# Optimization experiments

Hardware: AMD Instinct MI355X
Metric: run time of the kernel (lower is better)

The kernel has to match this reference:

```python
import jax, jax.numpy as jnp
import numpy as np

B, S, H, W, L = 32, 512, 768, 256, 8  # batch, subword seq, hidden, max words, max group size
INTENT, SLOT = 26, 121


def setup_inputs() -> dict:
    key = jax.random.key(0)
    ks = jax.random.split(key, 16)
    sc = 0.02
    res_all = jax.random.normal(ks[0], (B, S, H), jnp.float32)
    res = jax.random.normal(ks[1], (B, H), jnp.float32)
    # group covers indices start..start+lens inclusive (lens+1 <= L elements)
    token_start_idxs = jax.random.randint(ks[2], (B, W), 0, S - L, jnp.int32)
    subword_lengths = jax.random.randint(ks[3], (B, W), 1, L, jnp.int32)  # 1..7
    return {
        'res_all': res_all,
        'res': res,
        'token_start_idxs': token_start_idxs,
        'subword_lengths': subword_lengths,
        'Wsq_w': jax.random.normal(ks[4], (H, H), jnp.float32) * sc,
        'Wsq_b': jnp.zeros((H,), jnp.float32),
        'Wsk_w': jax.random.normal(ks[5], (H, H), jnp.float32) * sc,
        'Wsk_b': jnp.zeros((H,), jnp.float32),
        'Wsv_w': jax.random.normal(ks[6], (H, H), jnp.float32) * sc,
        'Wsv_b': jnp.zeros((H,), jnp.float32),
        'lin_id_w': jax.random.normal(ks[7], (INTENT, H), jnp.float32) * sc,
        'lin_id_b': jnp.zeros((INTENT,), jnp.float32),
        'lin_slot_w': jax.random.normal(ks[8], (SLOT, H), jnp.float32) * sc,
        'lin_slot_b': jnp.zeros((SLOT,), jnp.float32),
    }


def reference(res_all, res, token_start_idxs, subword_lengths,
              Wsq_w, Wsq_b, Wsk_w, Wsk_b, Wsv_w, Wsv_b,
              lin_id_w, lin_id_b, lin_slot_w, lin_slot_b):
    # intent head on pooled output
    res_id = res @ lin_id_w.T + lin_id_b  # [B, INTENT]

    # gather padded subword groups: torch.range is inclusive -> lens+1 subwords
    offs = jnp.arange(L, dtype=jnp.int32)                        # [L]
    idx = token_start_idxs[:, :, None] + offs[None, None, :]     # [B, W, L]
    idx = jnp.clip(idx, 0, S - 1)
    group = res_all[jnp.arange(B)[:, None, None], idx]           # [B, W, L, H]
    valid = offs[None, None, :] <= subword_lengths[:, :, None]   # [B, W, L], lens+1 valid

    # SAA_Attn: only the first row's attention output is used
    q0 = group[:, :, 0, :] @ Wsq_w.T + Wsq_b                     # [B, W, H]
    K = group @ Wsk_w.T + Wsk_b                                  # [B, W, L, H]
    V = group @ Wsv_w.T + Wsv_b                                  # [B, W, L, H]
    scores = jnp.einsum('bwh,bwkh->bwk', q0, K)                  # [B, W, L]
    scores = jnp.where(valid, scores, jnp.float32(-1e9))
    attn = jax.nn.softmax(scores, axis=-1)
    first = group[:, :, 0, :]
    attn_word = jnp.einsum('bwk,bwkh->bwh', attn, V) + first     # [B, W, H]

    # lens == 1 branch bypasses attention entirely
    word = jnp.where((subword_lengths == 1)[:, :, None], first, attn_word)

    res_sf = word @ lin_slot_w.T + lin_slot_b                    # [B, W, SLOT]
    return res_id, res_sf
```

## Files before the change

### kernel.cpp

```cpp
#include <hip/hip_runtime.h>
#include <cstdint>
#include <cstddef>

#define BB 32
#define SS 512
#define HH 768
#define WW 256
#define LL 8
#define NINTENT 26
#define NSLOT 121

typedef float f32x4 __attribute__((ext_vector_type(4)));
typedef __bf16 bf16x8 __attribute__((ext_vector_type(8)));

static __device__ __forceinline__ float bf2f(unsigned short u) {
    union { unsigned int i; float f; } x; x.i = ((unsigned int)u) << 16; return x.f;
}
static __device__ __forceinline__ unsigned short f2bf(float f) {
    union { float f; unsigned int i; } x; x.f = f;
    unsigned int r = (x.i + 0x7fffu + ((x.i >> 16) & 1u)) >> 16;
    return (unsigned short)r;
}

static __device__ __forceinline__ void gload16(const void* g, void* l) {
    __builtin_amdgcn_global_load_lds(
        (const __attribute__((address_space(1))) void*)g,
        (__attribute__((address_space(3))) void*)l, 16, 0, 0);
}

#define MF(a, b, c) __builtin_amdgcn_mfma_f32_16x16x32_bf16((a), (b), (c), 0, 0, 0)

__global__ __launch_bounds__(256) void prep_w(
    const float* __restrict__ Wk, const float* __restrict__ Wq,
    const float* __restrict__ Wv, const float* __restrict__ Ws,
    const float* __restrict__ bq, const float* __restrict__ bv,
    unsigned short* __restrict__ WkT_hi, unsigned short* __restrict__ WkT_lo,
    unsigned short* __restrict__ WqT_hi, unsigned short* __restrict__ WqT_lo,
    unsigned short* __restrict__ WvT, unsigned short* __restrict__ Wcomb,
    float* __restrict__ u_part,
    float* __restrict__ wsbv_part)
{
    int bid = blockIdx.x;
    int t = threadIdx.x;

    if (bid < 432) {
        __shared__ float tl[64][65];
        int mb = bid / 144, tb = bid % 144;
        int tx = tb % 12, ty = tb / 12;
        const float* src = (mb == 0) ? Wk : (mb == 1) ? Wq : Wv;
        int rr = t >> 4, c4 = (t & 15) * 4;
#pragma unroll
        for (int j = 0; j < 4; j++) {
            float4 v = *reinterpret_cast<const float4*>(
                &src[(size_t)(ty * 64 + rr + 16 * j) * HH + tx * 64 + c4]);
            tl[rr + 16 * j][c4 + 0] = v.x; tl[rr + 16 * j][c4 + 1] = v.y;
            tl[rr + 16 * j][c4 + 2] = v.z; tl[rr + 16 * j][c4 + 3] = v.w;
        }
        __syncthreads();
        int il = t >> 4, o4 = (t & 15) * 4;
        unsigned short* dhi = (mb == 0) ? WkT_hi : (mb == 1) ? WqT_hi : WvT;
        unsigned short* dlo = (mb == 0) ? WkT_lo : WqT_lo;
#pragma unroll
        for (int j = 0; j < 4; j++) {
            int i = il + 16 * j;
            float v0 = tl[o4 + 0][i], v1 = tl[o4 + 1][i];
            float v2 = tl[o4 + 2][i], v3 = tl[o4 + 3][i];
            size_t off = (size_t)(tx * 64 + i) * HH + ty * 64 + o4;
            ushort4 h;
            h.x = f2bf(v0); h.y = f2bf(v1); h.z = f2bf(v2); h.w = f2bf(v3);
            *reinterpret_cast<ushort4*>(&dhi[off]) = h;
            if (mb < 2) {
                ushort4 l;
                l.x = f2bf(v0 - bf2f(h.x)); l.y = f2bf(v1 - bf2f(h.y));
                l.z = f2bf(v2 - bf2f(h.z)); l.w = f2bf(v3 - bf2f(h.w));
                *reinterpret_cast<ushort4*>(&dlo[off]) = l;
            }
        }
        if (mb == 0) {
            int c = t >> 2, q = t & 3;
            float s = 0.f;
#pragma unroll
            for (int r = 0; r < 16; r++)
                s += bq[ty * 64 + q * 16 + r] * tl[q * 16 + r][c];
            s += __shfl_xor(s, 1);
            s += __shfl_xor(s, 2);
            if (q == 0) u_part[ty * HH + tx * 64 + c] = s;
        }
    } else {
        __shared__ float wred[4];
        int bid2 = bid - 432;
        int idx = bid2 * 256 + t;
        int row = idx / HH, col = idx % HH;
        float v = (row < NSLOT) ? Ws[row * HH + col] : 0.f;
        Wcomb[row * 1536 + col] = f2bf(v);
        float pv = v * bv[col];
        int lane = t & 63, wave = t >> 6;
#pragma unroll
        for (int off = 32; off > 0; off >>= 1) pv += __shfl_xor(pv, off);
        if (lane == 0) wred[wave] = pv;
        __syncthreads();
        if (t == 0)
            wsbv_part[(bid2 % 3) * 128 + row] = wred[0] + wred[1] + wred[2] + wred[3];
    }
}

__global__ __launch_bounds__(256) void gemm_weights(
    const uint4* __restrict__ WkT_hi, const uint4* __restrict__ WkT_lo,
    const uint4* __restrict__ WqT_hi, const uint4* __restrict__ WqT_lo,
    const uint4* __restrict__ WvT, const uint4* __restrict__ Wcomb,
    const float* __restrict__ res_all, const int* __restrict__ starts,
    const float* __restrict__ res, const float* __restrict__ id_w,
    const float* __restrict__ id_b,
    float* __restrict__ Ppart,
    float* __restrict__ WRpart,
    unsigned short* __restrict__ slotA,
    float* __restrict__ out)
{
    __shared__ uint4 sA[512];
    __shared__ uint4 sB[512];
    int bid = blockIdx.x;
    int t = threadIdx.x;
    int lane = t & 63, wave = t >> 6;

    if (bid >= 2384) {
        int w = (bid - 2384) * 4 + wave;
        int bb = w / 26, o = w - bb * 26;
        const float* rrow = res + bb * HH + lane * 12;
        const float* wrow = id_w + o * HH + lane * 12;
        float s = 0.f;
#pragma unroll
        for (int c = 0; c < 3; c++) {
            float4 a = *reinterpret_cast<const float4*>(&rrow[c * 4]);
            float4 b = *reinterpret_cast<const float4*>(&wrow[c * 4]);
            s += a.x * b.x + a.y * b.y + a.z * b.z + a.w * b.w;
        }
#pragma unroll
        for (int off = 32; off > 0; off >>= 1) s += __shfl_xor(s, off);
        if (lane == 0) out[bb * NINTENT + o] = s + id_b[o];
        return;
    }
    if (bid >= 336) {
        int gw = (bid - 336) * 4 + wave;
        int b = gw >> 8;
        int s0 = starts[gw];
        const float* src = res_all + (size_t)(b * SS + s0) * HH + lane * 12;
        unsigned short* dst = slotA + (size_t)gw * 1536 + lane * 12;
#pragma unroll
        for (int c2 = 0; c2 < 3; c2++) {
            float4 v = *reinterpret_cast<const float4*>(&src[c2 * 4]);
            ushort4 o;
            o.x = f2bf(v.x); o.y = f2bf(v.y); o.z = f2bf(v.z); o.w = f2bf(v.w);
            *reinterpret_cast<ushort4*>(&dst[c2 * 4]) = o;
        }
        return;
    }

    int wm = wave >> 1, wn = wave & 1;
    int l16 = lane & 15, lk = lane >> 4;
    int srow = lane >> 2, schk = lane & 3;
    uint4* sA0 = &sA[wave * 128];
    uint4* sA1 = &sA[wave * 128 + 64];
    uint4* sB0 = &sB[wave * 128];
    uint4* sB1 = &sB[wave * 128 + 64];

    f32x4 acc[4][4] = {};

    if (bid < 288) {
        int tile = bid >> 3, ks = bid & 7;
        int mt = tile / 6, nt = tile % 6;
        int kb = ks * 12;
#pragma unroll
        for (int p = 0; p < 3; p++) {
            const uint4* Ab = (p == 1) ? WkT_lo : WkT_hi;
            const uint4* Bb = (p == 2) ? WqT_lo : WqT_hi;
            const uint4* Ag0 = Ab + (size_t)(mt * 128 + wave * 32 + srow) * 96 + kb + schk;
            const uint4* Ag1 = Ag0 + (size_t)16 * 96;
            const uint4* Bg0 = Bb + (size_t)(nt * 128 + wave * 32 + srow) * 96 + kb + schk;
            const uint4* Bg1 = Bg0 + (size_t)16 * 96;
            for (int k0 = 0; k0 < 12; k0 += 4) {
                gload16(Ag0 + k0, sA0); gload16(Ag1 + k0, sA1);
                gload16(Bg0 + k0, sB0); gload16(Bg1 + k0, sB1);
                __syncthreads();
                bf16x8 af[4], bfr[4];
#pragma unroll
                for (int i = 0; i < 4; i++)
                    af[i] = *reinterpret_cast<const bf16x8*>(&sA[(wm * 64 + i * 16 + l16) * 4 + lk]);
#pragma unroll
                for (int j = 0; j < 4; j++)
                    bfr[j] = *reinterpret_cast<const bf16x8*>(&sB[(wn * 64 + j * 16 + l16) * 4 + lk]);
#pragma unroll
                for (int i = 0; i < 4; i++)
#pragma unroll
                    for (int j = 0; j < 4; j++)
                        acc[i][j] = MF(af[i], bfr[j], acc[i][j]);
                __syncthreads();
            }
        }
        float* dst = Ppart + (size_t)ks * 589824;
#pragma unroll
        for (int i = 0; i < 4; i++)
#pragma unroll
            for (int j = 0; j < 4; j++) {
                int col = nt * 128 + wn * 64 + j * 16 + l16;
#pragma unroll
                for (int q = 0; q < 4; q++) {
                    int row = mt * 128 + wm * 64 + i * 16 + lk * 4 + q;
                    dst[(size_t)row * HH + col] = acc[i][j][q];
                }
            }
    } else {
        int idx = bid - 288;
        int nt = idx >> 3, ks = idx & 7;
        int kb = ks * 12;
        const uint4* Ag0 = Wcomb + (size_t)(wave * 32 + srow) * 192 + kb + schk;
        const uint4* Ag1 = Ag0 + (size_t)16 * 192;
        const uint4* Bg0 = WvT + (size_t)(nt * 128 + wave * 32 + srow) * 96 + kb + schk;
        const uint4* Bg1 = Bg0 + (size_t)16 * 96;
        for (int k0 = 0; k0 < 12; k0 += 4) {
            gload16(Ag0 + k0, sA0); gload16(Ag1 + k0, sA1);
            gload16(Bg0 + k0, sB0); gload16(Bg1 + k0, sB1);
            __syncthreads();
            bf16x8 af[4], bfr[4];
#pragma unroll
            for (int i = 0; i < 4; i++)
                af[i] = *reinterpret_cast<const bf16x8*>(&sA[(wm * 64 + i * 16 + l16) * 4 + lk]);
#pragma unroll
            for (int j = 0; j < 4; j++)
                bfr[j] = *reinterpret_cast<const bf16x8*>(&sB[(wn * 64 + j * 16 + l16) * 4 + lk]);
#pragma unroll
            for (int i = 0; i < 4; i++)
#pragma unroll
                for (int j = 0; j < 4; j++)
                    acc[i][j] = MF(af[i], bfr[j], acc[i][j]);
            __syncthreads();
        }
        float* dst = WRpart + (size_t)ks * 98304;
#pragma unroll
        for (int i = 0; i < 4; i++)
#pragma unroll
            for (int j = 0; j < 4; j++) {
                int col = nt * 128 + wn * 64 + j * 16 + l16;
#pragma unroll
                for (int q = 0; q < 4; q++) {
                    int row = wm * 64 + i * 16 + lk * 4 + q;
                    dst[(size_t)row * HH + col] = acc[i][j][q];
                }
            }
    }
}

__global__ __launch_bounds__(256) void psum_kernel(
    const float4* __restrict__ Ppart, ushort4* __restrict__ Pb,
    const float4* __restrict__ WRpart, unsigned short* __restrict__ Wcomb,
    const float* __restrict__ u_part, float* __restrict__ u,
    const float* __restrict__ wsbv_part, float* __restrict__ wsbv)
{
    int bid = blockIdx.x, t = threadIdx.x;
    if (bid < 576) {
        int i = bid * 256 + t;
        float4 s = Ppart[i];
#pragma unroll
        for (int k = 1; k < 8; k++) {
            float4 v = Ppart[(size_t)k * 147456 + i];
            s.x += v.x; s.y += v.y; s.z += v.z; s.w += v.w;
        }
        ushort4 o;
        o.x = f2bf(s.x); o.y = f2bf(s.y); o.z = f2bf(s.z); o.w = f2bf(s.w);
        Pb[i] = o;
    } else if (bid < 672) {
        int q = (bid - 576) * 256 + t;
        float4 s = WRpart[q];
#pragma unroll
        for (int k = 1; k < 8; k++) {
            float4 v = WRpart[(size_t)k * 24576 + q];
            s.x += v.x; s.y += v.y; s.z += v.z; s.w += v.w;
        }
        int row = q / 192, colq = q % 192;
        ushort4 o;
        o.x = f2bf(s.x); o.y = f2bf(s.y); o.z = f2bf(s.z); o.w = f2bf(s.w);
        *reinterpret_cast<ushort4*>(&Wcomb[row * 1536 + 768 + colq * 4]) = o;
    } else if (bid < 675) {
        int c = (bid - 672) * 256 + t;
        float s = 0.f;
#pragma unroll
        for (int ty = 0; ty < 12; ty++) s += u_part[ty * HH + c];
        u[c] = s;
    } else if (t < 128) {
        wsbv[t] = wsbv_part[t] + wsbv_part[128 + t] + wsbv_part[256 + t];
    }
}

__global__ __launch_bounds__(256) void gemm_qp_sl(
    const uint4* __restrict__ A,
    const uint4* __restrict__ Bm,
    const uint4* __restrict__ Wc,
    const float* __restrict__ u,
    float* __restrict__ qp,
    float* __restrict__ Cpart0)
{
    __shared__ uint4 sA[256];
    __shared__ uint4 sB[512];

    int bid = blockIdx.x;
    int t = threadIdx.x;
    int lane = t & 63, wave = t >> 6;
    int wm = wave >> 1, wn = wave & 1;
    int l16 = lane & 15, lk = lane >> 4;
    int srow = lane >> 2, schk = lane & 3;

    if (bid >= 768) {
        int mt = bid - 768;
        const uint4* Ag  = A + (size_t)(mt * 32 + wave * 16 + srow) * 192 + schk;
        const uint4* Bg0 = Wc + (size_t)(wave * 32 + srow) * 192 + schk;
        const uint4* Bg1 = Bg0 + (size_t)16 * 192;
        uint4* sB0 = &sB[wave * 128];
        uint4* sB1 = &sB[wave * 128 + 64];

        f32x4 acc[4] = {};
        for (int k0 = 0; k0 < 96; k0 += 4) {
            if (wave < 2) gload16(Ag + k0, &sA[wave * 64]);
            gload16(Bg0 + k0, sB0);
            gload16(Bg1 + k0, sB1);
            __syncthreads();
            bf16x8 af = *reinterpret_cast<const bf16x8*>(&sA[(wm * 16 + l16) * 4 + lk]);
            bf16x8 bfr[4];
#pragma unroll
            for (int j = 0; j < 4; j++)
                bfr[j] = *reinterpret_cast<const bf16x8*>(&sB[(wn * 64 + j * 16 + l16) * 4 + lk]);
#pragma unroll
            for (int j = 0; j < 4; j++)
                acc[j] = MF(af, bfr[j], acc[j]);
            __syncthreads();
        }
#pragma unroll
        for (int j = 0; j < 4; j++) {
            int col = wn * 64 + j * 16 + l16;
#pragma unroll
            for (int q = 0; q < 4; q++) {
                int row = mt * 32 + wm * 16 + lk * 4 + q;
                Cpart0[(size_t)row * 128 + col] = acc[j][q];
            }
        }
        return;
    }

    bid = (bid & 7) * 96 + (bid >> 3);
    int mt = bid / 6, nt = bid % 6;

    const uint4* Ag  = A + (size_t)(mt * 64 + wave * 16 + srow) * 192 + schk;
    const uint4* Bg0 = Bm + (size_t)(nt * 128 + wave * 32 + srow) * 96 + schk;
    const uint4* Bg1 = Bg0 + (size_t)16 * 96;
    uint4* sAp = &sA[wave * 64];
    uint4* sB0 = &sB[wave * 128];
    uint4* sB1 = &sB[wave * 128 + 64];

    f32x4 acc[2][4] = {};

    for (int k0 = 0; k0 < 96; k0 += 4) {
        gload16(Ag + k0, sAp);
        gload16(Bg0 + k0, sB0);
        gload16(Bg1 + k0, sB1);
        __syncthreads();
        bf16x8 af[2], bfr[4];
#pragma unroll
        for (int i = 0; i < 2; i++)
            af[i] = *reinterpret_cast<const bf16x8*>(&sA[(wm * 32 + i * 16 + l16) * 4 + lk]);
#pragma unroll
        for (int j = 0; j < 4; j++)
            bfr[j] = *reinterpret_cast<const bf16x8*>(&sB[(wn * 64 + j * 16 + l16) * 4 + lk]);
#pragma unroll
        for (int i = 0; i < 2; i++)
#pragma unroll
            for (int j = 0; j < 4; j++)
                acc[i][j] = MF(af[i], bfr[j], acc[i][j]);
        __syncthreads();
    }

#pragma unroll
    for (int i = 0; i < 2; i++)
#pragma unroll
        for (int j = 0; j < 4; j++) {
            int col = nt * 128 + wn * 64 + j * 16 + l16;
            float add = u[col];
#pragma unroll
            for (int q = 0; q < 4; q++) {
                int row = mt * 64 + wm * 32 + i * 16 + lk * 4 + q;
                qp[(size_t)row * HH + col] = acc[i][j][q] + add;
            }
        }
}

__global__ __launch_bounds__(256) void attn2_kernel(
    const float* __restrict__ qp,
    const float* __restrict__ res_all,
    const int* __restrict__ starts,
    const int* __restrict__ lens,
    unsigned short* __restrict__ slotA)
{
    int bid = blockIdx.x;
    bid = (bid & 7) * 256 + (bid >> 3);
    int gw = bid * 4 + (threadIdx.x >> 6);
    int lane = threadIdx.x & 63;
    int b = gw >> 8;
    int s0 = starts[gw];
    int sl = lens[gw];

    unsigned short* dst = slotA + (size_t)gw * 1536 + 768 + lane * 12;

    if (sl == 1) {
        ushort4 z = {0, 0, 0, 0};
#pragma unroll
        for (int c = 0; c < 3; c++) *reinterpret_cast<ushort4*>(&dst[c * 4]) = z;
        return;
    }

    const float* qrow = qp + (size_t)gw * HH + lane * 12;
    float q[12];
#pragma unroll
    for (int c = 0; c < 3; c++) {
        float4 v = *reinterpret_cast<const float4*>(&qrow[c * 4]);
        q[c * 4 + 0] = v.x; q[c * 4 + 1] = v.y; q[c * 4 + 2] = v.z; q[c * 4 + 3] = v.w;
    }

    float m = -1e30f, ssum = 0.f;
    float acc[12];
#pragma unroll
    for (int i = 0; i < 12; i++) acc[i] = 0.f;

    for (int k = 0; k < LL; k++) {
        if (k > sl) break;
        int s = s0 + k; if (s > SS - 1) s = SS - 1;
        const float* xr = res_all + (size_t)(b * SS + s) * HH + lane * 12;
        float x[12];
        float partial = 0.f;
#pragma unroll
        for (int c = 0; c < 3; c++) {
            float4 v = *reinterpret_cast<const float4*>(&xr[c * 4]);
            x[c * 4 + 0] = v.x; x[c * 4 + 1] = v.y;
            x[c * 4 + 2] = v.z; x[c * 4 + 3] = v.w;
            partial += q[c * 4 + 0] * v.x + q[c * 4 + 1] * v.y
                     + q[c * 4 + 2] * v.z + q[c * 4 + 3] * v.w;
        }
#pragma unroll
        for (int off = 32; off > 0; off >>= 1) partial += __shfl_xor(partial, off);

        float mnew = (partial > m) ? partial : m;
        float scale = __expf(m - mnew);
        float e = __expf(partial - mnew);
        ssum = ssum * scale + e;
#pragma unroll
        for (int i = 0; i < 12; i++) acc[i] = acc[i] * scale + e * x[i];
        m = mnew;
    }

    float inv = 1.f / ssum;
#pragma unroll
    for (int c = 0; c < 3; c++) {
        ushort4 o;
        o.x = f2bf(acc[c * 4 + 0] * inv); o.y = f2bf(acc[c * 4 + 1] * inv);
        o.z = f2bf(acc[c * 4 + 2] * inv); o.w = f2bf(acc[c * 4 + 3] * inv);
        *reinterpret_cast<ushort4*>(&dst[c * 4]) = o;
    }
}

__global__ __launch_bounds__(256) void gemm_slot_r(
    const uint4* __restrict__ A,
    const uint4* __restrict__ Bm,
    const float* __restrict__ Cpart0,
    const float* __restrict__ bias, const float* __restrict__ wsbv,
    const int* __restrict__ lens,
    float* __restrict__ outsf)
{
    __shared__ uint4 sA[128];
    __shared__ uint4 sB[512];

    int mt = blockIdx.x;
    int t = threadIdx.x;
    int lane = t & 63, wave = t >> 6;
    int wm = wave >> 1, wn = wave & 1;
    int l16 = lane & 15, lk = lane >> 4;
    int srow = lane >> 2, schk = lane & 3;

    const uint4* Ag  = A + (size_t)(mt * 32 + wave * 16 + srow) * 192 + 96 + schk;
    const uint4* Bg0 = Bm + (size_t)(wave * 32 + srow) * 192 + 96 + schk;
    const uint4* Bg1 = Bg0 + (size_t)16 * 192;
    uint4* sB0 = &sB[wave * 128];
    uint4* sB1 = &sB[wave * 128 + 64];

    f32x4 acc[4] = {};

    for (int k0 = 0; k0 < 96; k0 += 4) {
        if (wave < 2) gload16(Ag + k0, &sA[wave * 64]);
        gload16(Bg0 + k0, sB0);
        gload16(Bg1 + k0, sB1);
        __syncthreads();
        bf16x8 af = *reinterpret_cast<const bf16x8*>(&sA[(wm * 16 + l16) * 4 + lk]);
        bf16x8 bfr[4];
#pragma unroll
        for (int j = 0; j < 4; j++)
            bfr[j] = *reinterpret_cast<const bf16x8*>(&sB[(wn * 64 + j * 16 + l16) * 4 + lk]);
#pragma unroll
        for (int j = 0; j < 4; j++)
            acc[j] = MF(af, bfr[j], acc[j]);
        __syncthreads();
    }

#pragma unroll
    for (int j = 0; j < 4; j++) {
        int col = wn * 64 + j * 16 + l16;
        if (col < NSLOT) {
            float bc = bias[col], wv = wsbv[col];
#pragma unroll
            for (int q = 0; q < 4; q++) {
                int row = mt * 32 + wm * 16 + lk * 4 + q;
                float v = acc[j][q] + Cpart0[(size_t)row * 128 + col]
                        + bc + ((lens[row] > 1) ? wv : 0.f);
                outsf[(size_t)row * NSLOT + col] = v;
            }
        }
    }
}

extern "C" void kernel_launch(void* const* d_in, const int* in_sizes, int n_in,
                              void* d_out, int out_size, void* d_ws, size_t ws_size,
                              hipStream_t stream) {
    const float* res_all    = (const float*)d_in[0];
    const float* res        = (const float*)d_in[1];
    const int*   starts     = (const int*)d_in[2];
    const int*   lens       = (const int*)d_in[3];
    const float* Wsq_w      = (const float*)d_in[4];
    const float* Wsq_b      = (const float*)d_in[5];
    const float* Wsk_w      = (const float*)d_in[6];
    const float* Wsk_b      = (const float*)d_in[7];
    const float* Wsv_w      = (const float*)d_in[8];
    const float* Wsv_b      = (const float*)d_in[9];
    const float* lin_id_w   = (const float*)d_in[10];
    const float* lin_id_b   = (const float*)d_in[11];
    const float* lin_slot_w = (const float*)d_in[12];
    const float* lin_slot_b = (const float*)d_in[13];
    float* out = (float*)d_out;
    (void)Wsk_b;

    char* ws = (char*)d_ws;
    unsigned short* slotA     = (unsigned short*)(ws + 0);
    float*          qp        = (float*)(ws + 25165824);
    unsigned short* WkT_hi    = (unsigned short*)(ws + 50331648);
    unsigned short* WkT_lo    = (unsigned short*)(ws + 51511296);
    unsigned short* WqT_hi    = (unsigned short*)(ws + 52690944);
    unsigned short* WqT_lo    = (unsigned short*)(ws + 53870592);
    unsigned short* WvT       = (unsigned short*)(ws + 55050240);
    unsigned short* Pb        = (unsigned short*)(ws + 56229888);
    unsigned short* Wcomb     = (unsigned short*)(ws + 57409536);
    float*          u         = (float*)(ws + 57802752);
    float*          wsbv      = (float*)(ws + 57805824);
    float*          u_part    = (float*)(ws + 57806336);
    float*          wsbv_part = (float*)(ws + 57843200);
    float*          Ppart     = (float*)(ws + 57845760);
    float*          WRpart    = (float*)(ws + 76720128);
    float*          Cpart0    = (float*)(ws + 79865856);

    prep_w<<<816, 256, 0, stream>>>(
        Wsk_w, Wsq_w, Wsv_w, lin_slot_w, Wsq_b, Wsv_b,
        WkT_hi, WkT_lo, WqT_hi, WqT_lo, WvT, Wcomb,
        u_part, wsbv_part);

    gemm_weights<<<2592, 256, 0, stream>>>(
        (const uint4*)WkT_hi, (const uint4*)WkT_lo,
        (const uint4*)WqT_hi, (const uint4*)WqT_lo,
        (const uint4*)WvT, (const uint4*)Wcomb,
        res_all, starts, res, lin_id_w, lin_id_b,
        Ppart, WRpart, slotA, out);

    psum_kernel<<<676, 256, 0, stream>>>(
        (const float4*)Ppart, (ushort4*)Pb, (const float4*)WRpart, Wcomb,
        u_part, u, wsbv_part, wsbv);

    gemm_qp_sl<<<1024, 256, 0, stream>>>((const uint4*)slotA, (const uint4*)Pb,
                                         (const uint4*)Wcomb, u, qp, Cpart0);

    attn2_kernel<<<2048, 256, 0, stream>>>(qp, res_all, starts, lens, slotA);

    gemm_slot_r<<<256, 256, 0, stream>>>((const uint4*)slotA, (const uint4*)Wcomb,
                                         Cpart0, lin_slot_b, wsbv, lens, out + 832);
}
```

Before: 88.31 us.

## Shrink weight-GEMM tiles, move slot GEMM into psum kernel, store qp in bf16

The weight-precompute GEMM tiles drop from 128x128 to 64x64. This gives four times more blocks for better occupancy and load balance, at the cost of lower data reuse per block. The slot-projection partial GEMM moves out of the qp GEMM and into the psum kernel launch, so it runs alongside the reductions. The qp intermediate is now stored as bf16, which halves its write and read traffic but loses some query precision in the attention scores.

Result: slower. 92.66 us (+4.9%).

```diff
diff --git a/kernel.cpp b/kernel.cpp
--- a/kernel.cpp
+++ b/kernel.cpp
@@ -116,14 +116,14 @@
     unsigned short* __restrict__ slotA,
     float* __restrict__ out)
 {
-    __shared__ uint4 sA[512];
-    __shared__ uint4 sB[512];
+    __shared__ uint4 sA[256];
+    __shared__ uint4 sB[256];
     int bid = blockIdx.x;
     int t = threadIdx.x;
     int lane = t & 63, wave = t >> 6;
 
-    if (bid >= 2384) {
-        int w = (bid - 2384) * 4 + wave;
+    if (bid >= 3392) {
+        int w = (bid - 3392) * 4 + wave;
         int bb = w / 26, o = w - bb * 26;
         const float* rrow = res + bb * HH + lane * 12;
         const float* wrow = id_w + o * HH + lane * 12;
@@ -139,8 +139,8 @@
         if (lane == 0) out[bb * NINTENT + o] = s + id_b[o];
         return;
     }
-    if (bid >= 336) {
-        int gw = (bid - 336) * 4 + wave;
+    if (bid >= 1344) {
+        int gw = (bid - 1344) * 4 + wave;
         int b = gw >> 8;
         int s0 = starts[gw];
         const float* src = res_all + (size_t)(b * SS + s0) * HH + lane * 12;
@@ -158,91 +158,84 @@
     int wm = wave >> 1, wn = wave & 1;
     int l16 = lane & 15, lk = lane >> 4;
     int srow = lane >> 2, schk = lane & 3;
-    uint4* sA0 = &sA[wave * 128];
-    uint4* sA1 = &sA[wave * 128 + 64];
-    uint4* sB0 = &sB[wave * 128];
-    uint4* sB1 = &sB[wave * 128 + 64];
-
-    f32x4 acc[4][4] = {};
-
-    if (bid < 288) {
+
+    f32x4 acc[2][2] = {};
+
+    if (bid < 1152) {
         int tile = bid >> 3, ks = bid & 7;
-        int mt = tile / 6, nt = tile % 6;
+        int mt = tile / 12, nt = tile % 12;
         int kb = ks * 12;
 #pragma unroll
         for (int p = 0; p < 3; p++) {
             const uint4* Ab = (p == 1) ? WkT_lo : WkT_hi;
             const uint4* Bb = (p == 2) ? WqT_lo : WqT_hi;
-            const uint4* Ag0 = Ab + (size_t)(mt * 128 + wave * 32 + srow) * 96 + kb + schk;
-            const uint4* Ag1 = Ag0 + (size_t)16 * 96;
-            const uint4* Bg0 = Bb + (size_t)(nt * 128 + wave * 32 + srow) * 96 + kb + schk;
-            const uint4* Bg1 = Bg0 + (size_t)16 * 96;
+            const uint4* Ag = Ab + (size_t)(mt * 64 + wave * 16 + srow) * 96 + kb + schk;
+            const uint4* Bg = Bb + (size_t)(nt * 64 + wave * 16 + srow) * 96 + kb + schk;
             for (int k0 = 0; k0 < 12; k0 += 4) {
-                gload16(Ag0 + k0, sA0); gload16(Ag1 + k0, sA1);
-                gload16(Bg0 + k0, sB0); gload16(Bg1 + k0, sB1);
+                gload16(Ag + k0, &sA[wave * 64]);
+                gload16(Bg + k0, &sB[wave * 64]);
                 __syncthreads();
-                bf16x8 af[4], bfr[4];
-#pragma unroll
-                for (int i = 0; i < 4; i++)
-                    af[i] = *reinterpret_cast<const bf16x8*>(&sA[(wm * 64 + i * 16 + l16) * 4 + lk]);
-#pragma unroll
-                for (int j = 0; j < 4; j++)
-                    bfr[j] = *reinterpret_cast<const bf16x8*>(&sB[(wn * 64 + j * 16 + l16) * 4 + lk]);
-#pragma unroll
-                for (int i = 0; i < 4; i++)
-#pragma unroll
-                    for (int j = 0; j < 4; j++)
+                bf16x8 af[2], bfr[2];
+#pragma unroll
+                for (int i = 0; i < 2; i++)
+                    af[i] = *reinterpret_cast<const bf16x8*>(&sA[(wm * 32 + i * 16 + l16) * 4 + lk]);
+#pragma unroll
+                for (int j = 0; j < 2; j++)
+                    bfr[j] = *reinterpret_cast<const bf16x8*>(&sB[(wn * 32 + j * 16 + l16) * 4 + lk]);
+#pragma unroll
+                for (int i = 0; i < 2; i++)
+#pragma unroll
+                    for (int j = 0; j < 2; j++)
                         acc[i][j] = MF(af[i], bfr[j], acc[i][j]);
                 __syncthreads();
             }
         }
         float* dst = Ppart + (size_t)ks * 589824;
 #pragma unroll
-        for (int i = 0; i < 4; i++)
-#pragma unroll
-            for (int j = 0; j < 4; j++) {
-                int col = nt * 128 + wn * 64 + j * 16 + l16;
+        for (int i = 0; i < 2; i++)
+#pragma unroll
+            for (int j = 0; j < 2; j++) {
+                int col = nt * 64 + wn * 32 + j * 16 + l16;
 #pragma unroll
                 for (int q = 0; q < 4; q++) {
-                    int row = mt * 128 + wm * 64 + i * 16 + lk * 4 + q;
+                    int row = mt * 64 + wm * 32 + i * 16 + lk * 4 + q;
                     dst[(size_t)row * HH + col] = acc[i][j][q];
                 }
             }
     } else {
-        int idx = bid - 288;
-        int nt = idx >> 3, ks = idx & 7;
+        int idx = bid - 1152;
+        int tile = idx >> 3, ks = idx & 7;
+        int mt = tile / 12, nt = tile % 12;
         int kb = ks * 12;
-        const uint4* Ag0 = Wcomb + (size_t)(wave * 32 + srow) * 192 + kb + schk;
-        const uint4* Ag1 = Ag0 + (size_t)16 * 192;
-        const uint4* Bg0 = WvT + (size_t)(nt * 128 + wave * 32 + srow) * 96 + kb + schk;
-        const uint4* Bg1 = Bg0 + (size_t)16 * 96;
+        const uint4* Ag = Wcomb + (size_t)(mt * 64 + wave * 16 + srow) * 192 + kb + schk;
+        const uint4* Bg = WvT + (size_t)(nt * 64 + wave * 16 + srow) * 96 + kb + schk;
         for (int k0 = 0; k0 < 12; k0 += 4) {
-            gload16(Ag0 + k0, sA0); gload16(Ag1 + k0, sA1);
-            gload16(Bg0 + k0, sB0); gload16(Bg1 + k0, sB1);
+            gload16(Ag + k0, &sA[wave * 64]);
+            gload16(Bg + k0, &sB[wave * 64]);
             __syncthreads();
-            bf16x8 af[4], bfr[4];
-#pragma unroll
-            for (int i = 0; i < 4; i++)
-                af[i] = *reinterpret_cast<const bf16x8*>(&sA[(wm * 64 + i * 16 + l16) * 4 + lk]);
-#pragma unroll
-            for (int j = 0; j < 4; j++)
-                bfr[j] = *reinterpret_cast<const bf16x8*>(&sB[(wn * 64 + j * 16 + l16) * 4 + lk]);
-#pragma unroll
-            for (int i = 0; i < 4; i++)
-#pragma unroll
-                for (int j = 0; j < 4; j++)
+            bf16x8 af[2], bfr[2];
+#pragma unroll
+            for (int i = 0; i < 2; i++)
+                af[i] = *reinterpret_cast<const bf16x8*>(&sA[(wm * 32 + i * 16 + l16) * 4 + lk]);
+#pragma unroll
+            for (int j = 0; j < 2; j++)
+                bfr[j] = *reinterpret_cast<const bf16x8*>(&sB[(wn * 32 + j * 16 + l16) * 4 + lk]);
+#pragma unroll
+            for (int i = 0; i < 2; i++)
+#pragma unroll
+                for (int j = 0; j < 2; j++)
                     acc[i][j] = MF(af[i], bfr[j], acc[i][j]);
             __syncthreads();
         }
         float* dst = WRpart + (size_t)ks * 98304;
 #pragma unroll
-        for (int i = 0; i < 4; i++)
-#pragma unroll
-            for (int j = 0; j < 4; j++) {
-                int col = nt * 128 + wn * 64 + j * 16 + l16;
+        for (int i = 0; i < 2; i++)
+#pragma unroll
+            for (int j = 0; j < 2; j++) {
+                int col = nt * 64 + wn * 32 + j * 16 + l16;
 #pragma unroll
                 for (int q = 0; q < 4; q++) {
-                    int row = wm * 64 + i * 16 + lk * 4 + q;
+                    int row = mt * 64 + wm * 32 + i * 16 + lk * 4 + q;
                     dst[(size_t)row * HH + col] = acc[i][j][q];
                 }
             }
@@ -253,8 +246,13 @@
     const float4* __restrict__ Ppart, ushort4* __restrict__ Pb,
     const float4* __restrict__ WRpart, unsigned short* __restrict__ Wcomb,
     const float* __restrict__ u_part, float* __restrict__ u,
-    const float* __restrict__ wsbv_part, float* __restrict__ wsbv)
+    const float* __restrict__ wsbv_part, float* __restrict__ wsbv,
+    const uint4* __restrict__ A,
+    const uint4* __restrict__ Wc,
+    float* __restrict__ Cpart0)
 {
+    __shared__ uint4 sA[128];
+    __shared__ uint4 sB[512];
     int bid = blockIdx.x, t = threadIdx.x;
     if (bid < 576) {
         int i = bid * 256 + t;
@@ -285,31 +283,16 @@
 #pragma unroll
         for (int ty = 0; ty < 12; ty++) s += u_part[ty * HH + c];
         u[c] = s;
-    } else if (t < 128) {
-        wsbv[t] = wsbv_part[t] + wsbv_part[128 + t] + wsbv_part[256 + t];
-    }
-}
-
-__global__ __launch_bounds__(256) void gemm_qp_sl(
-    const uint4* __restrict__ A,
-    const uint4* __restrict__ Bm,
-    const uint4* __restrict__ Wc,
-    const float* __restrict__ u,
-    float* __restrict__ qp,
-    float* __restrict__ Cpart0)
-{
-    __shared__ uint4 sA[256];
-    __shared__ uint4 sB[512];
-
-    int bid = blockIdx.x;
-    int t = threadIdx.x;
-    int lane = t & 63, wave = t >> 6;
-    int wm = wave >> 1, wn = wave & 1;
-    int l16 = lane & 15, lk = lane >> 4;
-    int srow = lane >> 2, schk = lane & 3;
-
-    if (bid >= 768) {
-        int mt = bid - 768;
+    } else if (bid == 675) {
+        if (t < 128)
+            wsbv[t] = wsbv_part[t] + wsbv_part[128 + t] + wsbv_part[256 + t];
+    } else {
+        int mt = bid - 676;
+        int lane = t & 63, wave = t >> 6;
+        int wm = wave >> 1, wn = wave & 1;
+        int l16 = lane & 15, lk = lane >> 4;
+        int srow = lane >> 2, schk = lane & 3;
+
         const uint4* Ag  = A + (size_t)(mt * 32 + wave * 16 + srow) * 192 + schk;
         const uint4* Bg0 = Wc + (size_t)(wave * 32 + srow) * 192 + schk;
         const uint4* Bg1 = Bg0 + (size_t)16 * 192;
@@ -341,11 +324,27 @@
                 Cpart0[(size_t)row * 128 + col] = acc[j][q];
             }
         }
-        return;
-    }
-
+    }
+}
+
+__global__ __launch_bounds__(256) void gemm_qp(
+    const uint4* __restrict__ A,
+    const uint4* __restrict__ Bm,
+    const float* __restrict__ u,
+    unsigned short* __restrict__ qp)
+{
+    __shared__ uint4 sA[256];
+    __shared__ uint4 sB[512];
+
+    int bid = blockIdx.x;
     bid = (bid & 7) * 96 + (bid >> 3);
     int mt = bid / 6, nt = bid % 6;
+
+    int t = threadIdx.x;
+    int lane = t & 63, wave = t >> 6;
+    int wm = wave >> 1, wn = wave & 1;
+    int l16 = lane & 15, lk = lane >> 4;
+    int srow = lane >> 2, schk = lane & 3;
 
     const uint4* Ag  = A + (size_t)(mt * 64 + wave * 16 + srow) * 192 + schk;
     const uint4* Bg0 = Bm + (size_t)(nt * 128 + wave * 32 + srow) * 96 + schk;
@@ -385,13 +384,13 @@
 #pragma unroll
             for (int q = 0; q < 4; q++) {
                 int row = mt * 64 + wm * 32 + i * 16 + lk * 4 + q;
-                qp[(size_t)row * HH + col] = acc[i][j][q] + add;
+                qp[(size_t)row * HH + col] = f2bf(acc[i][j][q] + add);
             }
         }
 }
 
 __global__ __launch_bounds__(256) void attn2_kernel(
-    const float* __restrict__ qp,
+    const unsigned short* __restrict__ qp,
     const float* __restrict__ res_all,
     const int* __restrict__ starts,
     const int* __restrict__ lens,
@@ -414,12 +413,13 @@
         return;
     }
 
-    const float* qrow = qp + (size_t)gw * HH + lane * 12;
+    const unsigned short* qrow = qp + (size_t)gw * HH + lane * 12;
     float q[12];
 #pragma unroll
     for (int c = 0; c < 3; c++) {
-        float4 v = *reinterpret_cast<const float4*>(&qrow[c * 4]);
-        q[c * 4 + 0] = v.x; q[c * 4 + 1] = v.y; q[c * 4 + 2] = v.z; q[c * 4 + 3] = v.w;
+        ushort4 v = *reinterpret_cast<const ushort4*>(&qrow[c * 4]);
+        q[c * 4 + 0] = bf2f(v.x); q[c * 4 + 1] = bf2f(v.y);
+        q[c * 4 + 2] = bf2f(v.z); q[c * 4 + 3] = bf2f(v.w);
     }
 
     float m = -1e30f, ssum = 0.f;
@@ -543,7 +543,7 @@
 
     char* ws = (char*)d_ws;
     unsigned short* slotA     = (unsigned short*)(ws + 0);
-    float*          qp        = (float*)(ws + 25165824);
+    unsigned short* qp        = (unsigned short*)(ws + 25165824);
     unsigned short* WkT_hi    = (unsigned short*)(ws + 50331648);
     unsigned short* WkT_lo    = (unsigned short*)(ws + 51511296);
     unsigned short* WqT_hi    = (unsigned short*)(ws + 52690944);
@@ -564,19 +564,19 @@
         WkT_hi, WkT_lo, WqT_hi, WqT_lo, WvT, Wcomb,
         u_part, wsbv_part);
 
-    gemm_weights<<<2592, 256, 0, stream>>>(
+    gemm_weights<<<3600, 256, 0, stream>>>(
         (const uint4*)WkT_hi, (const uint4*)WkT_lo,
         (const uint4*)WqT_hi, (const uint4*)WqT_lo,
         (const uint4*)WvT, (const uint4*)Wcomb,
         res_all, starts, res, lin_id_w, lin_id_b,
         Ppart, WRpart, slotA, out);
 
-    psum_kernel<<<676, 256, 0, stream>>>(
+    psum_kernel<<<932, 256, 0, stream>>>(
         (const float4*)Ppart, (ushort4*)Pb, (const float4*)WRpart, Wcomb,
-        u_part, u, wsbv_part, wsbv);
-
-    gemm_qp_sl<<<1024, 256, 0, stream>>>((const uint4*)slotA, (const uint4*)Pb,
-                                         (const uint4*)Wcomb, u, qp, Cpart0);
+        u_part, u, wsbv_part, wsbv,
+        (const uint4*)slotA, (const uint4*)Wcomb, Cpart0);
+
+    gemm_qp<<<768, 256, 0, stream>>>((const uint4*)slotA, (const uint4*)Pb, u, qp);
 
     attn2_kernel<<<2048, 256, 0, stream>>>(qp, res_all, starts, lens, slotA);
 
```
